# Performance work log

Measured on AMD Instinct MI355X. Metric: run time of the kernel, lower is better.

Reference implementation:

```python
import jax, jax.numpy as jnp
import numpy as np

B, S, ENC, DEC = 32, 2048, 1024, 1024
NEG = -1e10


def setup_inputs() -> dict:
    key = jax.random.key(0)
    k1, k2, k3, k4, k5, k6 = jax.random.split(key, 6)
    scale = 1.0 / np.sqrt(ENC + DEC)
    return {
        "hidden": jax.random.normal(k1, (B, DEC), dtype=jnp.float32),
        "encoder_outputs": jax.random.normal(k2, (B, S, ENC), dtype=jnp.float32),
        "mask": jax.random.randint(k3, (B, S), 0, 2, dtype=jnp.int32),
        "attn_w": jax.random.normal(k4, (DEC, ENC + DEC), dtype=jnp.float32) * scale,
        "attn_b": jax.random.normal(k5, (DEC,), dtype=jnp.float32) * scale,
        "v_w": jax.random.normal(k6, (DEC,), dtype=jnp.float32) * (1.0 / np.sqrt(DEC)),
    }


def reference(hidden, encoder_outputs, mask, attn_w, attn_b, v_w):
    # Split attn weight into hidden-part and encoder-part to avoid materializing the concat.
    w_h = attn_w[:, :DEC]    # [dec, dec]
    w_e = attn_w[:, DEC:]    # [dec, enc]
    # hidden is broadcast across src_len: [b, dec] -> contributes [b, 1, dec]
    h_proj = jnp.einsum('bd,kd->bk', hidden, w_h)[:, None, :]          # [b, 1, dec]
    e_proj = jnp.einsum('bse,ke->bsk', encoder_outputs, w_e)           # [b, s, dec]
    energy = jnp.tanh(h_proj + e_proj + attn_b)                        # [b, s, dec]
    attention = jnp.einsum('bsk,k->bs', energy, v_w)                   # [b, s]
    attention = jnp.where(mask == 0, NEG, attention)
    attention_weights = jax.nn.softmax(attention, axis=1)              # [b, s]
    context = jnp.einsum('bs,bse->be', attention_weights, encoder_outputs)
    return context, attention_weights
```

## Files before the change

kernel.cpp:

```cpp
#include <hip/hip_runtime.h>
#include <hip/hip_bf16.h>

#define NEG_ (-1e10f)

typedef short bf16x8 __attribute__((ext_vector_type(8)));
typedef float f32x4 __attribute__((ext_vector_type(4)));

__device__ __forceinline__ unsigned int pack_bf16x2(float a, float b) {
    __hip_bfloat162 h = __float22bfloat162_rn(make_float2(a, b));
    union { __hip_bfloat162 h2; unsigned int u; } cv;
    cv.h2 = h;
    return cv.u;
}

__device__ __forceinline__ void gload_lds16(const void* g, void* lds) {
    __builtin_amdgcn_global_load_lds(
        (const __attribute__((address_space(1))) unsigned int*)g,
        (__attribute__((address_space(3))) unsigned int*)lds,
        16, 0, 0);
}

__global__ __launch_bounds__(256) void cvt_enc_kernel(const float* __restrict__ enc,
                                                      unsigned int* __restrict__ encbf ) {
    const int tid = blockIdx.x * 256 + threadIdx.x;
#pragma unroll
    for (int i = 0; i < 8; ++i) {
        const size_t c = (size_t)tid + (size_t)i * 1048576;
        const float4 a0 = *reinterpret_cast<const float4*>(enc + c * 8);
        const float4 a1 = *reinterpret_cast<const float4*>(enc + c * 8 + 4);
        uint4 u = {pack_bf16x2(a0.x, a0.y), pack_bf16x2(a0.z, a0.w),
                   pack_bf16x2(a1.x, a1.y), pack_bf16x2(a1.z, a1.w)};
        *reinterpret_cast<uint4*>(encbf + c * 4) = u;
    }
}

__global__ __launch_bounds__(256) void cvt_w_kernel(const float* __restrict__ attn_w,
                                                    unsigned int* __restrict__ wbf) {
    const int idx = blockIdx.x * 256 + threadIdx.x;
    const int row = idx >> 7;
    const int c   = (idx & 127) * 8;
    const float* src = attn_w + (size_t)row * 2048 + 1024 + c;
    const float4 a0 = *reinterpret_cast<const float4*>(src);
    const float4 a1 = *reinterpret_cast<const float4*>(src + 4);
    uint4 u = {pack_bf16x2(a0.x, a0.y), pack_bf16x2(a0.z, a0.w),
               pack_bf16x2(a1.x, a1.y), pack_bf16x2(a1.z, a1.w)};
    *reinterpret_cast<uint4*>(wbf + (size_t)row * 512 + c / 2) = u;
}

__global__ __launch_bounds__(256) void hproj_kernel(const float* __restrict__ hidden,
                                                    const float* __restrict__ attn_w,
                                                    const float* __restrict__ attn_b,
                                                    float* __restrict__ hb) {
    __shared__ float row[1024];
    const int k = blockIdx.x;
    const int t = threadIdx.x;
    *reinterpret_cast<float4*>(&row[t * 4]) =
        *reinterpret_cast<const float4*>(&attn_w[(size_t)k * 2048 + t * 4]);
    __syncthreads();
    const int w = t >> 6, l = t & 63;
    const float bias = attn_b[k];
    for (int bi = 0; bi < 8; ++bi) {
        const int b = w * 8 + bi;
        const float* hrow = hidden + b * 1024;
        float p = 0.f;
#pragma unroll
        for (int i = 0; i < 16; ++i) p += hrow[l + 64 * i] * row[l + 64 * i];
#pragma unroll
        for (int off = 32; off > 0; off >>= 1) p += __shfl_xor(p, off);
        if (l == 0) hb[b * 1024 + k] = p + bias;
    }
}

__global__ __launch_bounds__(256, 3) void energy_gemm_kernel(const __hip_bfloat16* __restrict__ Abf,
                                                             const __hip_bfloat16* __restrict__ Bbf,
                                                             const float* __restrict__ hb,
                                                             const float* __restrict__ v_w,
                                                             float* __restrict__ logits) {
    __shared__ short As[128 * 64];
    __shared__ short Bs[128 * 64];

    const int t    = threadIdx.x;
    const int lane = t & 63;
    const int w    = t >> 6;
    const int wm   = w >> 1, wn = w & 1;

    const int logical = (blockIdx.x & 7) * 512 + (blockIdx.x >> 3);
    const int mi = logical >> 3, ni = logical & 7;
    const size_t m0 = (size_t)mi * 128;
    const int n0 = ni * 128;
    const int b  = mi >> 4;

    f32x4 acc[4][4];
#pragma unroll
    for (int i = 0; i < 4; ++i)
#pragma unroll
        for (int j = 0; j < 4; ++j) acc[i][j] = f32x4{0.f, 0.f, 0.f, 0.f};

    const char* Asrc = (const char*)Abf + ((m0 + w * 32 + (lane >> 3)) * 1024 + 0) * 2 + (lane & 7) * 16;
    const char* Bsrc = (const char*)Bbf + (((size_t)n0 + w * 32 + (lane >> 3)) * 1024) * 2 + (lane & 7) * 16;
    char* AsBase = (char*)As + w * 4096;
    char* BsBase = (char*)Bs + w * 4096;

    for (int kt = 0; kt < 16; ++kt) {
        const size_t ko = (size_t)kt * 128;
        __syncthreads();
#pragma unroll
        for (int i = 0; i < 4; ++i) {
            gload_lds16(Asrc + (size_t)i * 8 * 2048 + ko, AsBase + i * 1024);
            gload_lds16(Bsrc + (size_t)i * 8 * 2048 + ko, BsBase + i * 1024);
        }
        __syncthreads();
#pragma unroll
        for (int ks = 0; ks < 2; ++ks) {
            bf16x8 af[4], bfr[4];
            const int cbyte = ks * 64 + (lane >> 4) * 16;
#pragma unroll
            for (int fm = 0; fm < 4; ++fm)
                af[fm] = *reinterpret_cast<const bf16x8*>(
                    (const char*)As + (wm * 64 + fm * 16 + (lane & 15)) * 128 + cbyte);
#pragma unroll
            for (int fn = 0; fn < 4; ++fn)
                bfr[fn] = *reinterpret_cast<const bf16x8*>(
                    (const char*)Bs + (wn * 64 + fn * 16 + (lane & 15)) * 128 + cbyte);
#pragma unroll
            for (int fm = 0; fm < 4; ++fm)
#pragma unroll
                for (int fn = 0; fn < 4; ++fn)
                    acc[fm][fn] = __builtin_amdgcn_mfma_f32_16x16x32_bf16(
                        af[fm], bfr[fn], acc[fm][fn], 0, 0, 0);
        }
    }

    const int cl = lane & 15, rg = lane >> 4;
    float rs[4][4];
#pragma unroll
    for (int i = 0; i < 4; ++i)
#pragma unroll
        for (int j = 0; j < 4; ++j) rs[i][j] = 0.f;

#pragma unroll
    for (int fn = 0; fn < 4; ++fn) {
        const int n = n0 + wn * 64 + fn * 16 + cl;
        const float hbv = hb[b * 1024 + n];
        const float vwv = v_w[n];
#pragma unroll
        for (int fm = 0; fm < 4; ++fm) {
#pragma unroll
            for (int r = 0; r < 4; ++r) {
                float x  = acc[fm][fn][r] + hbv;
                float x2 = fminf(fmaxf(2.f * x, -80.f), 80.f);
                float ex = __expf(x2);
                float th = 1.f - 2.f / (ex + 1.f);
                rs[fm][r] += th * vwv;
            }
        }
    }
#pragma unroll
    for (int fm = 0; fm < 4; ++fm) {
#pragma unroll
        for (int r = 0; r < 4; ++r) {
            float v = rs[fm][r];
            v += __shfl_xor(v, 1);
            v += __shfl_xor(v, 2);
            v += __shfl_xor(v, 4);
            v += __shfl_xor(v, 8);
            if (cl == 0)
                atomicAdd(&logits[m0 + wm * 64 + fm * 16 + rg * 4 + r], v);
        }
    }
}

__global__ __launch_bounds__(256) void softmax_kernel(const float* __restrict__ logits,
                                                      const int* __restrict__ mask,
                                                      float* __restrict__ wout) {
    const int b = blockIdx.x, t = threadIdx.x;
    __shared__ float red[4];
    float v[8];
    float m = -3.4e38f;
#pragma unroll
    for (int i = 0; i < 8; ++i) {
        const int s = t + i * 256;
        float x = logits[b * 2048 + s];
        if (mask[b * 2048 + s] == 0) x = NEG_;
        v[i] = x;
        m = fmaxf(m, x);
    }
#pragma unroll
    for (int off = 32; off > 0; off >>= 1) m = fmaxf(m, __shfl_xor(m, off));
    if ((t & 63) == 0) red[t >> 6] = m;
    __syncthreads();
    m = fmaxf(fmaxf(red[0], red[1]), fmaxf(red[2], red[3]));
    __syncthreads();
    float sum = 0.f;
#pragma unroll
    for (int i = 0; i < 8; ++i) {
        v[i] = __expf(v[i] - m);
        sum += v[i];
    }
#pragma unroll
    for (int off = 32; off > 0; off >>= 1) sum += __shfl_xor(sum, off);
    if ((t & 63) == 0) red[t >> 6] = sum;
    __syncthreads();
    sum = red[0] + red[1] + red[2] + red[3];
    const float inv = 1.f / sum;
#pragma unroll
    for (int i = 0; i < 8; ++i) wout[b * 2048 + t + i * 256] = v[i] * inv;
}

__global__ __launch_bounds__(256) void ctx_partial_kernel(const float* __restrict__ enc,
                                                          const float* __restrict__ wts,
                                                          float* __restrict__ part) {
    const int b  = blockIdx.x >> 6;
    const int sp = blockIdx.x & 63;
    const int t  = threadIdx.x;
    const float* wrow = wts + b * 2048 + sp * 32;
    const float* erow = enc + ((size_t)b * 2048 + sp * 32) * 1024 + t * 4;
    float4 acc = {0.f, 0.f, 0.f, 0.f};
#pragma unroll 8
    for (int s = 0; s < 32; ++s) {
        const float w = wrow[s];
        float4 e = *reinterpret_cast<const float4*>(erow + (size_t)s * 1024);
        acc.x += w * e.x; acc.y += w * e.y; acc.z += w * e.z; acc.w += w * e.w;
    }
    *reinterpret_cast<float4*>(&part[(size_t)blockIdx.x * 1024 + t * 4]) = acc;
}

__global__ __launch_bounds__(256) void ctx_reduce_kernel(const float* __restrict__ part,
                                                         float* __restrict__ ctx) {
    const int idx = blockIdx.x * 256 + threadIdx.x;
    const int b = idx >> 10, e = idx & 1023;
    float s = 0.f;
#pragma unroll
    for (int sp = 0; sp < 64; ++sp) s += part[(size_t)(b * 64 + sp) * 1024 + e];
    ctx[idx] = s;
}

extern "C" void kernel_launch(void* const* d_in, const int* in_sizes, int n_in,
                              void* d_out, int out_size, void* d_ws, size_t ws_size,
                              hipStream_t stream) {
    const float* hidden = (const float*)d_in[0];
    const float* enc    = (const float*)d_in[1];
    const int*   mask   = (const int*)d_in[2];
    const float* attn_w = (const float*)d_in[3];
    const float* attn_b = (const float*)d_in[4];
    const float* v_w    = (const float*)d_in[5];

    float* out = (float*)d_out;
    float* ctx = out;
    float* wts = out + 32 * 1024;

    char* ws = (char*)d_ws;
    __hip_bfloat16* encbf = (__hip_bfloat16*)ws;
    __hip_bfloat16* wbf   = (__hip_bfloat16*)(ws + 134217728);
    float* hb     = (float*)(ws + 134217728 + 2097152);
    float* logits = hb + 32 * 1024;
    float* part   = logits + 32 * 2048;

    hipMemsetAsync(logits, 0, 32 * 2048 * sizeof(float), stream);
    cvt_enc_kernel<<<4096, 256, 0, stream>>>(enc, (unsigned int*)encbf);
    cvt_w_kernel<<<512, 256, 0, stream>>>(attn_w, (unsigned int*)wbf);
    hproj_kernel<<<1024, 256, 0, stream>>>(hidden, attn_w, attn_b, hb);
    energy_gemm_kernel<<<4096, 256, 0, stream>>>(encbf, wbf, hb, v_w, logits);
    softmax_kernel<<<32, 256, 0, stream>>>(logits, mask, wts);
    ctx_partial_kernel<<<2048, 256, 0, stream>>>(enc, wts, part);
    ctx_reduce_kernel<<<128, 256, 0, stream>>>(part, ctx);
}
```

Before: 666.9 us.

## Swizzle GEMM LDS, fuse weight prep, read bf16 encoder in context with atomics

Merges the weight bf16 conversion into the h-projection kernel so attn_w is read once. Adds an XOR swizzle to the GEMM's LDS layout to avoid bank conflicts and raises the occupancy hint to 4. The context pass now reads the bf16 copy of the encoder instead of fp32, halving that traffic, and accumulates into the output with atomics, removing the partial buffer and reduce kernel. In exchange, context precision drops to bf16 inputs, and the atomic summation order is nondeterministic.

```diff
diff --git a/kernel.cpp b/kernel.cpp
--- a/kernel.cpp
+++ b/kernel.cpp
@@ -13,6 +13,12 @@
     return cv.u;
 }
 
+__device__ __forceinline__ float b2f(short s) {
+    union { float f; unsigned u; } c;
+    c.u = ((unsigned)(unsigned short)s) << 16;
+    return c.f;
+}
+
 __device__ __forceinline__ void gload_lds16(const void* g, void* lds) {
     __builtin_amdgcn_global_load_lds(
         (const __attribute__((address_space(1))) unsigned int*)g,
@@ -21,7 +27,7 @@
 }
 
 __global__ __launch_bounds__(256) void cvt_enc_kernel(const float* __restrict__ enc,
-                                                      unsigned int* __restrict__ encbf ) {
+                                                      unsigned int* __restrict__ encbf) {
     const int tid = blockIdx.x * 256 + threadIdx.x;
 #pragma unroll
     for (int i = 0; i < 8; ++i) {
@@ -34,29 +40,24 @@
     }
 }
 
-__global__ __launch_bounds__(256) void cvt_w_kernel(const float* __restrict__ attn_w,
-                                                    unsigned int* __restrict__ wbf) {
-    const int idx = blockIdx.x * 256 + threadIdx.x;
-    const int row = idx >> 7;
-    const int c   = (idx & 127) * 8;
-    const float* src = attn_w + (size_t)row * 2048 + 1024 + c;
-    const float4 a0 = *reinterpret_cast<const float4*>(src);
-    const float4 a1 = *reinterpret_cast<const float4*>(src + 4);
-    uint4 u = {pack_bf16x2(a0.x, a0.y), pack_bf16x2(a0.z, a0.w),
-               pack_bf16x2(a1.x, a1.y), pack_bf16x2(a1.z, a1.w)};
-    *reinterpret_cast<uint4*>(wbf + (size_t)row * 512 + c / 2) = u;
-}
-
-__global__ __launch_bounds__(256) void hproj_kernel(const float* __restrict__ hidden,
+__global__ __launch_bounds__(256) void wprep_kernel(const float* __restrict__ hidden,
                                                     const float* __restrict__ attn_w,
                                                     const float* __restrict__ attn_b,
-                                                    float* __restrict__ hb) {
-    __shared__ float row[1024];
+                                                    float* __restrict__ hb,
+                                                    unsigned int* __restrict__ wbf) {
+    __shared__ float row[2048];
     const int k = blockIdx.x;
     const int t = threadIdx.x;
-    *reinterpret_cast<float4*>(&row[t * 4]) =
-        *reinterpret_cast<const float4*>(&attn_w[(size_t)k * 2048 + t * 4]);
-    __syncthreads();
+    *reinterpret_cast<float4*>(&row[t * 8]) =
+        *reinterpret_cast<const float4*>(&attn_w[(size_t)k * 2048 + t * 8]);
+    *reinterpret_cast<float4*>(&row[t * 8 + 4]) =
+        *reinterpret_cast<const float4*>(&attn_w[(size_t)k * 2048 + t * 8 + 4]);
+    __syncthreads();
+    {
+        const float* s = &row[1024 + t * 4];
+        uint2 u = {pack_bf16x2(s[0], s[1]), pack_bf16x2(s[2], s[3])};
+        *reinterpret_cast<uint2*>(wbf + (size_t)k * 512 + t * 2) = u;
+    }
     const int w = t >> 6, l = t & 63;
     const float bias = attn_b[k];
     for (int bi = 0; bi < 8; ++bi) {
@@ -71,7 +72,7 @@
     }
 }
 
-__global__ __launch_bounds__(256, 3) void energy_gemm_kernel(const __hip_bfloat16* __restrict__ Abf,
+__global__ __launch_bounds__(256, 4) void energy_gemm_kernel(const __hip_bfloat16* __restrict__ Abf,
                                                              const __hip_bfloat16* __restrict__ Bbf,
                                                              const float* __restrict__ hb,
                                                              const float* __restrict__ v_w,
@@ -96,10 +97,13 @@
 #pragma unroll
         for (int j = 0; j < 4; ++j) acc[i][j] = f32x4{0.f, 0.f, 0.f, 0.f};
 
-    const char* Asrc = (const char*)Abf + ((m0 + w * 32 + (lane >> 3)) * 1024 + 0) * 2 + (lane & 7) * 16;
-    const char* Bsrc = (const char*)Bbf + (((size_t)n0 + w * 32 + (lane >> 3)) * 1024) * 2 + (lane & 7) * 16;
+    const int csrc = (((lane & 7) ^ (lane >> 3)) * 16);
+    const char* Asrc = (const char*)Abf + (m0 + w * 32 + (lane >> 3)) * 2048 + csrc;
+    const char* Bsrc = (const char*)Bbf + ((size_t)n0 + w * 32 + (lane >> 3)) * 2048 + csrc;
     char* AsBase = (char*)As + w * 4096;
     char* BsBase = (char*)Bs + w * 4096;
+
+    const int swz = lane & 7;
 
     for (int kt = 0; kt < 16; ++kt) {
         const size_t ko = (size_t)kt * 128;
@@ -113,15 +117,15 @@
 #pragma unroll
         for (int ks = 0; ks < 2; ++ks) {
             bf16x8 af[4], bfr[4];
-            const int cbyte = ks * 64 + (lane >> 4) * 16;
+            const int cb = ((ks * 4 + (lane >> 4)) ^ swz) * 16;
 #pragma unroll
             for (int fm = 0; fm < 4; ++fm)
                 af[fm] = *reinterpret_cast<const bf16x8*>(
-                    (const char*)As + (wm * 64 + fm * 16 + (lane & 15)) * 128 + cbyte);
+                    (const char*)As + (wm * 64 + fm * 16 + (lane & 15)) * 128 + cb);
 #pragma unroll
             for (int fn = 0; fn < 4; ++fn)
                 bfr[fn] = *reinterpret_cast<const bf16x8*>(
-                    (const char*)Bs + (wn * 64 + fn * 16 + (lane & 15)) * 128 + cbyte);
+                    (const char*)Bs + (wn * 64 + fn * 16 + (lane & 15)) * 128 + cb);
 #pragma unroll
             for (int fm = 0; fm < 4; ++fm)
 #pragma unroll
@@ -207,32 +211,27 @@
     for (int i = 0; i < 8; ++i) wout[b * 2048 + t + i * 256] = v[i] * inv;
 }
 
-__global__ __launch_bounds__(256) void ctx_partial_kernel(const float* __restrict__ enc,
+__global__ __launch_bounds__(256) void ctx_partial_kernel(const __hip_bfloat16* __restrict__ encbf,
                                                           const float* __restrict__ wts,
-                                                          float* __restrict__ part) {
+                                                          float* __restrict__ ctx) {
     const int b  = blockIdx.x >> 6;
     const int sp = blockIdx.x & 63;
     const int t  = threadIdx.x;
     const float* wrow = wts + b * 2048 + sp * 32;
-    const float* erow = enc + ((size_t)b * 2048 + sp * 32) * 1024 + t * 4;
+    const char* base = (const char*)encbf + ((size_t)b * 2048 + sp * 32) * 2048 + t * 8;
     float4 acc = {0.f, 0.f, 0.f, 0.f};
 #pragma unroll 8
     for (int s = 0; s < 32; ++s) {
-        const float w = wrow[s];
-        float4 e = *reinterpret_cast<const float4*>(erow + (size_t)s * 1024);
-        acc.x += w * e.x; acc.y += w * e.y; acc.z += w * e.z; acc.w += w * e.w;
-    }
-    *reinterpret_cast<float4*>(&part[(size_t)blockIdx.x * 1024 + t * 4]) = acc;
-}
-
-__global__ __launch_bounds__(256) void ctx_reduce_kernel(const float* __restrict__ part,
-                                                         float* __restrict__ ctx) {
-    const int idx = blockIdx.x * 256 + threadIdx.x;
-    const int b = idx >> 10, e = idx & 1023;
-    float s = 0.f;
-#pragma unroll
-    for (int sp = 0; sp < 64; ++sp) s += part[(size_t)(b * 64 + sp) * 1024 + e];
-    ctx[idx] = s;
+        const float wv = wrow[s];
+        short4 e = *reinterpret_cast<const short4*>(base + (size_t)s * 2048);
+        acc.x += wv * b2f(e.x); acc.y += wv * b2f(e.y);
+        acc.z += wv * b2f(e.z); acc.w += wv * b2f(e.w);
+    }
+    float* dst = ctx + b * 1024 + t * 4;
+    atomicAdd(dst + 0, acc.x);
+    atomicAdd(dst + 1, acc.y);
+    atomicAdd(dst + 2, acc.z);
+    atomicAdd(dst + 3, acc.w);
 }
 
 extern "C" void kernel_launch(void* const* d_in, const int* in_sizes, int n_in,
@@ -254,14 +253,12 @@
     __hip_bfloat16* wbf   = (__hip_bfloat16*)(ws + 134217728);
     float* hb     = (float*)(ws + 134217728 + 2097152);
     float* logits = hb + 32 * 1024;
-    float* part   = logits + 32 * 2048;
 
     hipMemsetAsync(logits, 0, 32 * 2048 * sizeof(float), stream);
+    hipMemsetAsync(ctx, 0, 32 * 1024 * sizeof(float), stream);
     cvt_enc_kernel<<<4096, 256, 0, stream>>>(enc, (unsigned int*)encbf);
-    cvt_w_kernel<<<512, 256, 0, stream>>>(attn_w, (unsigned int*)wbf);
-    hproj_kernel<<<1024, 256, 0, stream>>>(hidden, attn_w, attn_b, hb);
+    wprep_kernel<<<1024, 256, 0, stream>>>(hidden, attn_w, attn_b, hb, (unsigned int*)wbf);
     energy_gemm_kernel<<<4096, 256, 0, stream>>>(encbf, wbf, hb, v_w, logits);
     softmax_kernel<<<32, 256, 0, stream>>>(logits, mask, wts);
-    ctx_partial_kernel<<<2048, 256, 0, stream>>>(enc, wts, part);
-    ctx_reduce_kernel<<<128, 256, 0, stream>>>(part, ctx);
-}
+    ctx_partial_kernel<<<2048, 256, 0, stream>>>(encbf, wts, ctx);
+}
```

New measurement: 605.5 us. -9.2%, faster.
